# Optimization experiments

Measured on AMD Instinct MI355X. Metric: run time of the kernel, lower is better.

The kernel has to match this reference:

```python
import jax, jax.numpy as jnp
import numpy as np

B, S, D = 2, 2048, 4096
H, KVH, HD = 32, 8, 128
THETA = 10000.0


def setup_inputs() -> dict:
    key = jax.random.key(0)
    k1, k2, k3 = jax.random.split(key, 3)
    hidden_states = jax.random.normal(k1, (B, S, D), jnp.float32)
    w_qkv = jax.random.normal(k2, ((KVH * 2 + H) * HD, D), jnp.float32) * 0.02
    w_dense = jax.random.normal(k3, (D, D), jnp.float32) * 0.02
    return {"hidden_states": hidden_states, "w_qkv": w_qkv, "w_dense": w_dense}


def _rope(x, pos):
    # x: [B, H, S, HD]; Falcon rotary embedding (rotate_half convention)
    inv_freq = 1.0 / (THETA ** (jnp.arange(0, HD, 2, dtype=jnp.float32) / HD))
    freqs = pos[:, None] * inv_freq[None, :]           # [S, HD/2]
    emb = jnp.concatenate([freqs, freqs], axis=-1)      # [S, HD]
    cos, sin = jnp.cos(emb), jnp.sin(emb)
    x1, x2 = x[..., : HD // 2], x[..., HD // 2 :]
    rot = jnp.concatenate([-x2, x1], axis=-1)
    return x * cos + rot * sin


def reference(hidden_states, w_qkv, w_dense):
    # fused QKV projection (FalconLinear, no bias)
    fused = jnp.einsum('bsd,ed->bse', hidden_states, w_qkv)  # [B,S,(2KVH+H)*HD]
    g = H // KVH  # query heads per kv head
    qkv = fused.reshape(B, S, KVH, g + 2, HD)
    q = qkv[:, :, :, :g]                        # [B,S,KVH,g,HD]
    k = jnp.broadcast_to(qkv[:, :, :, g:g + 1], q.shape)
    v = jnp.broadcast_to(qkv[:, :, :, g + 1:g + 2], q.shape)
    q, k, v = (t.reshape(B, S, H, HD).transpose(0, 2, 1, 3) for t in (q, k, v))
    pos = jnp.arange(S, dtype=jnp.float32)
    q = _rope(q, pos)
    k = _rope(k, pos)
    scores = jnp.einsum('bhqd,bhkd->bhqk', q, k) / jnp.sqrt(jnp.float32(HD))
    causal = jnp.tril(jnp.ones((S, S), dtype=bool))
    scores = jnp.where(causal, scores, jnp.float32(-1e9))
    attn = jax.nn.softmax(scores, axis=-1)
    out = jnp.einsum('bhqk,bhkd->bhqd', attn, v)
    out = out.transpose(0, 2, 1, 3).reshape(B, S, H * HD)   # merge heads
    return jnp.einsum('bsd,ed->bse', out, w_dense)
```

## Files before the change

### kernel.cpp

```cpp
#include <hip/hip_runtime.h>

#define B_   2
#define S_   2048
#define D_   4096
#define H_   32
#define KVH_ 8
#define HD_  128
#define NE_  6144

using f32x4  = __attribute__((ext_vector_type(4))) float;
using bf16x8 = __attribute__((ext_vector_type(8))) __bf16;
using u16x8  = __attribute__((ext_vector_type(8))) unsigned short;

__device__ __forceinline__ unsigned short f2bf(float f) {
  union { float f; unsigned u; } v; v.f = f;
  unsigned r = v.u + 0x7FFFu + ((v.u >> 16) & 1u);
  return (unsigned short)(r >> 16);
}
__device__ __forceinline__ float bf2f(unsigned short h) {
  union { unsigned u; float f; } v; v.u = ((unsigned)h) << 16; return v.f;
}
__device__ __forceinline__ bf16x8 ld8(const unsigned short* p) {
  return *reinterpret_cast<const bf16x8*>(p);
}
__device__ __forceinline__ bf16x8 ld8b(const void* base, int byte_off) {
  return *reinterpret_cast<const bf16x8*>((const char*)base + byte_off);
}
__device__ __forceinline__ void cp16(const void* g, void* l) {
  __builtin_amdgcn_global_load_lds(
      (const __attribute__((address_space(1))) void*)g,
      (__attribute__((address_space(3))) void*)l, 16, 0, 0);
}
__device__ __forceinline__ float exp2a(float x) {
  float r; asm("v_exp_f32 %0, %1" : "=v"(r) : "v"(x)); return r;
}

__global__ __launch_bounds__(256) void cvt_f32_bf16(
    const float* __restrict__ in, unsigned short* __restrict__ out, int n4)
{
  int i = blockIdx.x * 256 + threadIdx.x;
  if (i >= n4) return;
  f32x4 v = *reinterpret_cast<const f32x4*>(in + (size_t)i * 4);
  ushort4 o;
  o.x = f2bf(v[0]); o.y = f2bf(v[1]); o.z = f2bf(v[2]); o.w = f2bf(v[3]);
  *reinterpret_cast<ushort4*>(out + (size_t)i * 4) = o;
}

__global__ __launch_bounds__(256) void cvt2_f32_bf16(
    const float* __restrict__ s0, unsigned short* __restrict__ d0, int n0,
    const float* __restrict__ s1, unsigned short* __restrict__ d1, int n1)
{
  int i = blockIdx.x * 256 + threadIdx.x;
  const float* src; unsigned short* dst;
  if (i < n0) { src = s0; dst = d0; }
  else        { i -= n0; if (i >= n1) return; src = s1; dst = d1; }
  f32x4 v = *reinterpret_cast<const f32x4*>(src + (size_t)i * 4);
  ushort4 o;
  o.x = f2bf(v[0]); o.y = f2bf(v[1]); o.z = f2bf(v[2]); o.w = f2bf(v[3]);
  *reinterpret_cast<ushort4*>(dst + (size_t)i * 4) = o;
}

template <typename OutT, int NT>
__global__ __launch_bounds__(512, 2) void gemm256(
    const unsigned short* __restrict__ A,
    const unsigned short* __restrict__ Bw,
    OutT* __restrict__ C, int M, int N)
{
  constexpr int K  = 4096;
  constexpr int NI = (K / 64) / 2;
  constexpr int NB = NT / 64;
  constexpr int NN = NT / 64;
  constexpr int WN = NT / 4;
  constexpr int BBUF = NT * 128;
  __shared__ __align__(16) char lds[65536 + 2 * BBUF];

  const int tid  = threadIdx.x;
  const int lane = tid & 63;
  const int wave = tid >> 6;
  const int wr = wave >> 2;
  const int wc = wave & 3;
  const int lr = lane & 15;
  const int lk = (lane >> 4) * 8;

  int id  = blockIdx.y * gridDim.x + blockIdx.x;
  const int nwg = gridDim.x * gridDim.y;
  if ((nwg & 7) == 0) { const int q = nwg >> 3; id = (id & 7) * q + (id >> 3); }
  const int row0 = (id / gridDim.x) * 256;
  const int col0 = (id % gridDim.x) * NT;

  int rwA[2], csA[2], dbA[2];
#pragma unroll
  for (int j = 0; j < 2; ++j) {
    dbA[j] = j * 8192 + tid * 16;
    rwA[j] = dbA[j] >> 7;
    csA[j] = ((dbA[j] & 127) ^ ((rwA[j] & 7) << 4)) >> 1;
  }
  auto stA = [&](int buf, int h, int t) {
#pragma unroll
    for (int j = 0; j < 2; ++j)
      cp16(A + (size_t)(row0 + h * 128 + rwA[j]) * K + t * 64 + csA[j],
           lds + buf * 32768 + h * 16384 + dbA[j]);
  };
  const int dbB = tid * 16;
  const int rwB = dbB >> 7;
  const int csB = ((dbB & 127) ^ ((rwB & 7) << 4)) >> 1;
  auto stB = [&](int buf, int c, int t) {
    cp16(Bw + (size_t)(col0 + c * 64 + rwB) * K + t * 64 + csB,
         lds + 65536 + buf * BBUF + c * 8192 + dbB);
  };

  const int cb0 = ((0 + lk) << 1) ^ ((lr & 7) << 4);
  const int cb1 = ((32 + lk) << 1) ^ ((lr & 7) << 4);
  const int aRowB = (wr * 128 + lr) * 128;
  const int bRowB = (wc * WN + lr) * 128;

  f32x4 acc[8][NN];
#pragma unroll
  for (int m = 0; m < 8; ++m)
#pragma unroll
    for (int n = 0; n < NN; ++n) acc[m][n] = (f32x4){0.f, 0.f, 0.f, 0.f};
  bf16x8 bfr[NN][2];

#define FENCE asm volatile("" ::: "memory")
#define VMNB  do { if constexpr (NB == 4) asm volatile("s_waitcnt vmcnt(4)" ::: "memory"); \
                   else                   asm volatile("s_waitcnt vmcnt(3)" ::: "memory"); } while (0)
#define VM0   asm volatile("s_waitcnt vmcnt(0)" ::: "memory")

#define PHASE(p, buf, STAGE, WAIT)                                             \
  {                                                                            \
    if ((p) == 0) {                                                            \
      _Pragma("unroll")                                                        \
      for (int n = 0; n < NN; ++n) {                                           \
        bfr[n][0] = ld8b(lds, 65536 + (buf) * BBUF + bRowB + n * 2048 + cb0);  \
        bfr[n][1] = ld8b(lds, 65536 + (buf) * BBUF + bRowB + n * 2048 + cb1);  \
      }                                                                        \
    }                                                                          \
    bf16x8 a00 = ld8b(lds, (buf) * 32768 + aRowB + ((p) * 2 + 0) * 2048 + cb0);\
    bf16x8 a01 = ld8b(lds, (buf) * 32768 + aRowB + ((p) * 2 + 0) * 2048 + cb1);\
    bf16x8 a10 = ld8b(lds, (buf) * 32768 + aRowB + ((p) * 2 + 1) * 2048 + cb0);\
    bf16x8 a11 = ld8b(lds, (buf) * 32768 + aRowB + ((p) * 2 + 1) * 2048 + cb1);\
    STAGE;                                                                     \
    FENCE;                                                                     \
    __builtin_amdgcn_s_barrier();                                              \
    __builtin_amdgcn_s_setprio(1);                                             \
    _Pragma("unroll")                                                          \
    for (int n = 0; n < NN; ++n) {                                             \
      acc[(p)*2+0][n] = __builtin_amdgcn_mfma_f32_16x16x32_bf16(a00, bfr[n][0], acc[(p)*2+0][n], 0, 0, 0); \
      acc[(p)*2+0][n] = __builtin_amdgcn_mfma_f32_16x16x32_bf16(a01, bfr[n][1], acc[(p)*2+0][n], 0, 0, 0); \
      acc[(p)*2+1][n] = __builtin_amdgcn_mfma_f32_16x16x32_bf16(a10, bfr[n][0], acc[(p)*2+1][n], 0, 0, 0); \
      acc[(p)*2+1][n] = __builtin_amdgcn_mfma_f32_16x16x32_bf16(a11, bfr[n][1], acc[(p)*2+1][n], 0, 0, 0); \
    }                                                                          \
    __builtin_amdgcn_s_setprio(0);                                             \
    WAIT;                                                                      \
    FENCE;                                                                     \
    __builtin_amdgcn_s_barrier();                                              \
  }

#pragma unroll
  for (int c = 0; c < NB; ++c) stB(0, c, 0);
  stA(0, 0, 0); stA(0, 1, 0);
#pragma unroll
  for (int c = 0; c < NB; ++c) stB(1, c, 1);
  VMNB;
  FENCE;
  __builtin_amdgcn_s_barrier();

  for (int i = 0; i < NI; ++i) {
    const int t1  = 2 * i + 1;
    const int tn0 = 2 * i + 2;
    const int tn1 = 2 * i + 3;
    const bool pre = (i + 1 < NI);
    PHASE(0, 0, { stA(1, 0, t1); }, {});
    PHASE(1, 0, { stA(1, 1, t1); }, {});
    PHASE(2, 0, { if (pre) { stB(0, 0, tn0); stB(0, 1, tn0); } }, {});
    PHASE(3, 0, { if (pre) { _Pragma("unroll") for (int c = 2; c < NB; ++c) stB(0, c, tn0); } },
          { if (pre) { VMNB; } else { VM0; } });
    PHASE(0, 1, { if (pre) stA(0, 0, tn0); }, {});
    PHASE(1, 1, { if (pre) stA(0, 1, tn0); }, {});
    PHASE(2, 1, { if (pre) { stB(1, 0, tn1); stB(1, 1, tn1); } }, {});
    PHASE(3, 1, { if (pre) { _Pragma("unroll") for (int c = 2; c < NB; ++c) stB(1, c, tn1); } },
          { if (pre) { VMNB; } });
  }
#undef PHASE
#undef FENCE
#undef VMNB
#undef VM0

  const int orow = (lane >> 4) * 4;
#pragma unroll
  for (int m = 0; m < 8; ++m) {
    const int gr0 = row0 + wr * 128 + m * 16 + orow;
#pragma unroll
    for (int n = 0; n < NN; ++n) {
      const int gc = col0 + wc * WN + n * 16 + lr;
#pragma unroll
      for (int r = 0; r < 4; ++r) {
        float val = acc[m][n][r];
        if constexpr (sizeof(OutT) == 2)
          C[(size_t)(gr0 + r) * N + gc] = f2bf(val);
        else
          C[(size_t)(gr0 + r) * N + gc] = val;
      }
    }
  }
}

__global__ __launch_bounds__(256) void rope_scatter(
    const unsigned short* __restrict__ fused,
    unsigned short* __restrict__ Qr,
    unsigned short* __restrict__ Kr,
    unsigned short* __restrict__ Vt)
{
  int idx = blockIdx.x * 256 + threadIdx.x;
  int dg = idx & 7;
  int t = idx >> 3;
  int e = t % 48;
  int bs = t / 48;
  int s = bs % S_;
  int b = bs / S_;
  int kvh = e / 6, j = e % 6;
  const unsigned short* src = fused + (size_t)bs * NE_ + e * 128 + dg * 8;
  u16x8 lo = *reinterpret_cast<const u16x8*>(src);
  u16x8 hi = *reinterpret_cast<const u16x8*>(src + 64);
  if (j == 5) {
    size_t base = (size_t)(b * KVH_ + kvh) * HD_ * S_ + s;
#pragma unroll
    for (int jj = 0; jj < 8; ++jj) {
      Vt[base + (size_t)(dg * 8 + jj) * S_]      = lo[jj];
      Vt[base + (size_t)(dg * 8 + jj + 64) * S_] = hi[jj];
    }
  } else {
    u16x8 olo, ohi;
#pragma unroll
    for (int jj = 0; jj < 8; ++jj) {
      int d = dg * 8 + jj;
      float x1 = bf2f(lo[jj]), x2 = bf2f(hi[jj]);
      float inv = __expf(-(float)d * (9.2103403719761836f / 64.0f));
      float ang = (float)s * inv;
      float sn, c;
      sincosf(ang, &sn, &c);
      olo[jj] = f2bf(x1 * c - x2 * sn);
      ohi[jj] = f2bf(x2 * c + x1 * sn);
    }
    unsigned short* dst;
    if (j == 4) dst = Kr + ((size_t)(b * KVH_ + kvh) * S_ + s) * HD_;
    else        dst = Qr + ((size_t)(b * H_ + kvh * 4 + j) * S_ + s) * HD_;
    *reinterpret_cast<u16x8*>(dst + dg * 8)      = olo;
    *reinterpret_cast<u16x8*>(dst + dg * 8 + 64) = ohi;
  }
}

__global__ __launch_bounds__(256) void attn_fwd(
    const unsigned short* __restrict__ Qr,
    const unsigned short* __restrict__ Kr,
    const unsigned short* __restrict__ Vt,
    unsigned short* __restrict__ O)
{
  __shared__ __align__(16) unsigned short Kld[2][64 * 128];
  __shared__ __align__(16) unsigned short Vld[2][128 * 64];
  __shared__ __align__(16) unsigned short Pld[4][16 * 64];

  const int tid  = threadIdx.x;
  const int lane = tid & 63;
  const int wave = tid >> 6;
  const int bx = blockIdx.x;
  const int h  = blockIdx.y;
  const int b  = blockIdx.z;
  const int kvh = h >> 2;
  const int lr = lane & 15;
  const int lk = (lane >> 4) * 8;
  const int orow = (lane >> 4) * 4;

  const float SC2 = 0.08838834764831845f * 1.4426950408889634f;
  const unsigned short* Kb = Kr + (size_t)(b * KVH_ + kvh) * S_ * HD_;
  const unsigned short* Vb = Vt + (size_t)(b * KVH_ + kvh) * HD_ * S_;

  auto stage = [&](int buf, int kb) {
#pragma unroll
    for (int i = 0; i < 4; ++i) {
      const int db = i * 4096 + tid * 16;
      {
        const int row  = db >> 8;
        const int colb = (db & 255) ^ ((row & 7) << 4);
        cp16(Kb + (size_t)(kb * 64 + row) * HD_ + (colb >> 1),
             (char*)&Kld[buf][0] + i * 4096 + wave * 1024);
      }
      {
        const int row  = db >> 7;
        const int colb = (db & 127) ^ ((row & 7) << 4);
        cp16(Vb + (size_t)row * S_ + kb * 64 + (colb >> 1),
             (char*)&Vld[buf][0] + i * 4096 + wave * 1024);
      }
    }
  };

  for (int half = 0; half < 2; ++half) {
    const int qb = half ? (S_ / 64 - 1 - bx) : bx;

    const unsigned short* qbase =
        Qr + ((size_t)(b * H_ + h) * S_ + qb * 64 + wave * 16 + lr) * HD_;
    bf16x8 qf[4];
#pragma unroll
    for (int t = 0; t < 4; ++t) {
      union { bf16x8 v; unsigned short s2[8]; } u;
      u.v = ld8(qbase + t * 32 + lk);
#pragma unroll
      for (int jj = 0; jj < 8; ++jj) u.s2[jj] = f2bf(bf2f(u.s2[jj]) * SC2);
      qf[t] = u.v;
    }

    f32x4 acc_o[8];
#pragma unroll
    for (int dt = 0; dt < 8; ++dt) acc_o[dt] = (f32x4){0.f, 0.f, 0.f, 0.f};
    float mrow[4], lpart[4];
#pragma unroll
    for (int r = 0; r < 4; ++r) { mrow[r] = -1e30f; lpart[r] = 0.f; }

    stage(0, 0);
    __syncthreads();

    for (int kb = 0; kb <= qb; ++kb) {
      const int cur = kb & 1;
      if (kb < qb) stage(cur ^ 1, kb + 1);

      const char* Kc = (const char*)&Kld[cur][0];
      const char* Vc = (const char*)&Vld[cur][0];

      f32x4 accs[4];
#pragma unroll
      for (int kt = 0; kt < 4; ++kt) accs[kt] = (f32x4){0.f, 0.f, 0.f, 0.f};
      __builtin_amdgcn_s_setprio(1);
#pragma unroll
      for (int t = 0; t < 4; ++t) {
#pragma unroll
        for (int kt = 0; kt < 4; ++kt) {
          const int krow = kt * 16 + lr;
          const int kbyte = ((krow << 8) + ((t * 32 + lk) << 1)) ^ ((krow & 7) << 4);
          bf16x8 kf = ld8b(Kc, kbyte);
          accs[kt] = __builtin_amdgcn_mfma_f32_16x16x32_bf16(qf[t], kf, accs[kt], 0, 0, 0);
        }
      }
      __builtin_amdgcn_s_setprio(0);

      if (kb == qb) {
#pragma unroll
        for (int r = 0; r < 4; ++r) {
          const int qg = wave * 16 + orow + r;
#pragma unroll
          for (int kt = 0; kt < 4; ++kt)
            if (kt * 16 + lr > qg) accs[kt][r] = -1e30f;
        }
      }

      float mx[4];
#pragma unroll
      for (int r = 0; r < 4; ++r)
        mx[r] = fmaxf(fmaxf(accs[0][r], accs[1][r]), fmaxf(accs[2][r], accs[3][r]));
      int ok = (mx[0] <= mrow[0] + 8.f) && (mx[1] <= mrow[1] + 8.f) &&
               (mx[2] <= mrow[2] + 8.f) && (mx[3] <= mrow[3] + 8.f);
      if (!__all(ok)) {
        float corr[4];
#pragma unroll
        for (int r = 0; r < 4; ++r) {
          float m = mx[r];
#pragma unroll
          for (int msk = 8; msk >= 1; msk >>= 1) m = fmaxf(m, __shfl_xor(m, msk, 64));
          float mnew = fmaxf(mrow[r], m);
          corr[r] = exp2a(mrow[r] - mnew);
          mrow[r] = mnew;
          lpart[r] *= corr[r];
        }
#pragma unroll
        for (int dt = 0; dt < 8; ++dt)
#pragma unroll
          for (int r = 0; r < 4; ++r) acc_o[dt][r] *= corr[r];
      }

#pragma unroll
      for (int r = 0; r < 4; ++r) {
        const int prow = orow + r;
#pragma unroll
        for (int kt = 0; kt < 4; ++kt) {
          float p = exp2a(accs[kt][r] - mrow[r]);
          lpart[r] += p;
          const int pbyte = ((prow << 7) + ((kt * 16 + lr) << 1)) ^ ((prow & 7) << 4);
          *(__bf16*)((char*)&Pld[wave][0] + pbyte) = (__bf16)p;
        }
      }

      asm volatile("" ::: "memory");

      __builtin_amdgcn_s_setprio(1);
#pragma unroll
      for (int kc = 0; kc < 2; ++kc) {
        const int pbyte = ((lr << 7) + ((kc * 32 + lk) << 1)) ^ ((lr & 7) << 4);
        bf16x8 pf = ld8b(&Pld[wave][0], pbyte);
#pragma unroll
        for (int dt = 0; dt < 8; ++dt) {
          const int vrow = dt * 16 + lr;
          const int vbyte = ((vrow << 7) + ((kc * 32 + lk) << 1)) ^ ((vrow & 7) << 4);
          bf16x8 vf = ld8b(Vc, vbyte);
          acc_o[dt] = __builtin_amdgcn_mfma_f32_16x16x32_bf16(pf, vf, acc_o[dt], 0, 0, 0);
        }
      }
      __builtin_amdgcn_s_setprio(0);

      __syncthreads();
    }

#pragma unroll
    for (int r = 0; r < 4; ++r) {
      float s = lpart[r];
#pragma unroll
      for (int msk = 8; msk >= 1; msk >>= 1) s += __shfl_xor(s, msk, 64);
      float inv = 1.f / s;
      size_t rowoff =
          (size_t)(b * S_ + qb * 64 + wave * 16 + orow + r) * (H_ * HD_) + h * HD_;
#pragma unroll
      for (int dt = 0; dt < 8; ++dt)
        O[rowoff + dt * 16 + lr] = f2bf(acc_o[dt][r] * inv);
    }
  }
}

__global__ void fill_sentinel(float* __restrict__ O, int n) {
  int i = blockIdx.x * 256 + threadIdx.x;
  if (i < n) O[i] = 12345.0f;
}

extern "C" void kernel_launch(void* const* d_in, const int* in_sizes, int n_in,
                              void* d_out, int out_size, void* d_ws, size_t ws_size,
                              hipStream_t stream) {
  const float* hidden = (const float*)d_in[0];
  const float* wqkv   = (const float*)d_in[1];
  const float* wdense = (const float*)d_in[2];
  float* out = (float*)d_out;

  const size_t NEED = 134217728;
  if (ws_size < NEED) {
    fill_sentinel<<<dim3((out_size + 255) / 256), dim3(256), 0, stream>>>(out, out_size);
    return;
  }

  char* ws = (char*)d_ws;
  unsigned short* Hb    = (unsigned short*)(ws);
  unsigned short* Wqb   = (unsigned short*)(ws + 33554432);
  unsigned short* fused = (unsigned short*)(ws + 83886080);
  unsigned short* Qr    = (unsigned short*)(ws);
  unsigned short* Kr    = (unsigned short*)(ws + 33554432);
  unsigned short* Vt    = (unsigned short*)(ws + 41943040);
  unsigned short* Wdb   = (unsigned short*)(ws + 50331648);
  unsigned short* attn_out = (unsigned short*)(ws + 83886080);

  const int nH4 = B_ * S_ * D_ / 4;
  const int nQ4 = NE_ * D_ / 4;
  const int nD4 = D_ * D_ / 4;

  cvt2_f32_bf16<<<dim3((nH4 + nQ4 + 255) / 256), dim3(256), 0, stream>>>(
      hidden, Hb, nH4, wqkv, Wqb, nQ4);

  gemm256<unsigned short, 192><<<dim3(NE_ / 192, (B_ * S_) / 256), dim3(512), 0, stream>>>(
      Hb, Wqb, fused, B_ * S_, NE_);

  cvt_f32_bf16<<<dim3(nD4 / 256), dim3(256), 0, stream>>>(wdense, Wdb, nD4);

  rope_scatter<<<dim3((B_ * S_ * 48 * 8) / 256), dim3(256), 0, stream>>>(
      fused, Qr, Kr, Vt);

  attn_fwd<<<dim3(16, H_, B_), dim3(256), 0, stream>>>(Qr, Kr, Vt, attn_out);

  gemm256<float, 256><<<dim3(D_ / 256, (B_ * S_) / 256), dim3(512), 0, stream>>>(
      attn_out, Wdb, out, B_ * S_, D_);
}
```

Before: 524.1 us.

## Fuse dense-weight conversion into RoPE kernel, fold Q scaling, reorder GEMM staging

Measured after the change: 527.0 us. About the same (+0.6%).

```diff
diff --git a/kernel.cpp b/kernel.cpp
--- a/kernel.cpp
+++ b/kernel.cpp
@@ -35,16 +35,7 @@
   float r; asm("v_exp_f32 %0, %1" : "=v"(r) : "v"(x)); return r;
 }
 
-__global__ __launch_bounds__(256) void cvt_f32_bf16(
-    const float* __restrict__ in, unsigned short* __restrict__ out, int n4)
-{
-  int i = blockIdx.x * 256 + threadIdx.x;
-  if (i >= n4) return;
-  f32x4 v = *reinterpret_cast<const f32x4*>(in + (size_t)i * 4);
-  ushort4 o;
-  o.x = f2bf(v[0]); o.y = f2bf(v[1]); o.z = f2bf(v[2]); o.w = f2bf(v[3]);
-  *reinterpret_cast<ushort4*>(out + (size_t)i * 4) = o;
-}
+#define SC2F 0.12751652f
 
 __global__ __launch_bounds__(256) void cvt2_f32_bf16(
     const float* __restrict__ s0, unsigned short* __restrict__ d0, int n0,
@@ -170,16 +161,14 @@
     const int tn0 = 2 * i + 2;
     const int tn1 = 2 * i + 3;
     const bool pre = (i + 1 < NI);
-    PHASE(0, 0, { stA(1, 0, t1); }, {});
-    PHASE(1, 0, { stA(1, 1, t1); }, {});
-    PHASE(2, 0, { if (pre) { stB(0, 0, tn0); stB(0, 1, tn0); } }, {});
-    PHASE(3, 0, { if (pre) { _Pragma("unroll") for (int c = 2; c < NB; ++c) stB(0, c, tn0); } },
-          { if (pre) { VMNB; } else { VM0; } });
-    PHASE(0, 1, { if (pre) stA(0, 0, tn0); }, {});
-    PHASE(1, 1, { if (pre) stA(0, 1, tn0); }, {});
-    PHASE(2, 1, { if (pre) { stB(1, 0, tn1); stB(1, 1, tn1); } }, {});
-    PHASE(3, 1, { if (pre) { _Pragma("unroll") for (int c = 2; c < NB; ++c) stB(1, c, tn1); } },
-          { if (pre) { VMNB; } });
+    PHASE(0, 0, { stA(1, 0, t1); stA(1, 1, t1); }, {});
+    PHASE(1, 0, { if (pre) { stB(0, 0, tn0); stB(0, 1, tn0); } }, {});
+    PHASE(2, 0, { if (pre) { _Pragma("unroll") for (int c = 2; c < NB; ++c) stB(0, c, tn0); } }, {});
+    PHASE(3, 0, {}, { if (pre) { VMNB; } else { VM0; } });
+    PHASE(0, 1, { if (pre) { stA(0, 0, tn0); stA(0, 1, tn0); } }, {});
+    PHASE(1, 1, { if (pre) { stB(1, 0, tn1); stB(1, 1, tn1); } }, {});
+    PHASE(2, 1, { if (pre) { _Pragma("unroll") for (int c = 2; c < NB; ++c) stB(1, c, tn1); } }, {});
+    PHASE(3, 1, {}, { if (pre) { VMNB; } });
   }
 #undef PHASE
 #undef FENCE
@@ -205,13 +194,26 @@
   }
 }
 
-__global__ __launch_bounds__(256) void rope_scatter(
+#define ROPE_N (B_ * S_ * 48 * 8)
+__global__ __launch_bounds__(256) void rope_scatter_cvt(
     const unsigned short* __restrict__ fused,
     unsigned short* __restrict__ Qr,
     unsigned short* __restrict__ Kr,
-    unsigned short* __restrict__ Vt)
+    unsigned short* __restrict__ Vt,
+    const float* __restrict__ wdense,
+    unsigned short* __restrict__ Wdb,
+    int nD4)
 {
   int idx = blockIdx.x * 256 + threadIdx.x;
+  if (idx >= ROPE_N) {
+    int i = idx - ROPE_N;
+    if (i >= nD4) return;
+    f32x4 v = *reinterpret_cast<const f32x4*>(wdense + (size_t)i * 4);
+    ushort4 o;
+    o.x = f2bf(v[0]); o.y = f2bf(v[1]); o.z = f2bf(v[2]); o.w = f2bf(v[3]);
+    *reinterpret_cast<ushort4*>(Wdb + (size_t)i * 4) = o;
+    return;
+  }
   int dg = idx & 7;
   int t = idx >> 3;
   int e = t % 48;
@@ -230,6 +232,7 @@
       Vt[base + (size_t)(dg * 8 + jj + 64) * S_] = hi[jj];
     }
   } else {
+    const float sc = (j == 4) ? 1.0f : SC2F;
     u16x8 olo, ohi;
 #pragma unroll
     for (int jj = 0; jj < 8; ++jj) {
@@ -239,8 +242,8 @@
       float ang = (float)s * inv;
       float sn, c;
       sincosf(ang, &sn, &c);
-      olo[jj] = f2bf(x1 * c - x2 * sn);
-      ohi[jj] = f2bf(x2 * c + x1 * sn);
+      olo[jj] = f2bf((x1 * c - x2 * sn) * sc);
+      ohi[jj] = f2bf((x2 * c + x1 * sn) * sc);
     }
     unsigned short* dst;
     if (j == 4) dst = Kr + ((size_t)(b * KVH_ + kvh) * S_ + s) * HD_;
@@ -271,7 +274,6 @@
   const int lk = (lane >> 4) * 8;
   const int orow = (lane >> 4) * 4;
 
-  const float SC2 = 0.08838834764831845f * 1.4426950408889634f;
   const unsigned short* Kb = Kr + (size_t)(b * KVH_ + kvh) * S_ * HD_;
   const unsigned short* Vb = Vt + (size_t)(b * KVH_ + kvh) * HD_ * S_;
 
@@ -301,13 +303,7 @@
         Qr + ((size_t)(b * H_ + h) * S_ + qb * 64 + wave * 16 + lr) * HD_;
     bf16x8 qf[4];
 #pragma unroll
-    for (int t = 0; t < 4; ++t) {
-      union { bf16x8 v; unsigned short s2[8]; } u;
-      u.v = ld8(qbase + t * 32 + lk);
-#pragma unroll
-      for (int jj = 0; jj < 8; ++jj) u.s2[jj] = f2bf(bf2f(u.s2[jj]) * SC2);
-      qf[t] = u.v;
-    }
+    for (int t = 0; t < 4; ++t) qf[t] = ld8(qbase + t * 32 + lk);
 
     f32x4 acc_o[8];
 #pragma unroll
@@ -462,10 +458,8 @@
   gemm256<unsigned short, 192><<<dim3(NE_ / 192, (B_ * S_) / 256), dim3(512), 0, stream>>>(
       Hb, Wqb, fused, B_ * S_, NE_);
 
-  cvt_f32_bf16<<<dim3(nD4 / 256), dim3(256), 0, stream>>>(wdense, Wdb, nD4);
-
-  rope_scatter<<<dim3((B_ * S_ * 48 * 8) / 256), dim3(256), 0, stream>>>(
-      fused, Qr, Kr, Vt);
+  rope_scatter_cvt<<<dim3((ROPE_N + nD4 + 255) / 256), dim3(256), 0, stream>>>(
+      fused, Qr, Kr, Vt, wdense, Wdb, nD4);
 
   attn_fwd<<<dim3(16, H_, B_), dim3(256), 0, stream>>>(Qr, Kr, Vt, attn_out);
 
```
